# Kernel optimization log

Hardware: AMD Instinct MI355X
Metric: run time of the kernel (lower is better)

Reference implementation:

```python
import jax, jax.numpy as jnp
import numpy as np

NEG_INF = -1e30

def setup_inputs() -> dict:
    key0 = jax.random.key(0)
    kq, kk, kv, ks = jax.random.split(key0, 4)
    B, S, H, D = 4, 2048, 16, 128
    query = jax.random.normal(kq, (B, S, H, D), dtype=jnp.float32)
    key = jax.random.normal(kk, (B, S, H, D), dtype=jnp.float32)
    value = jax.random.normal(kv, (B, S, H, D), dtype=jnp.float32)
    decoder_segment_ids = jnp.sort(jax.random.randint(ks, (B, S), 0, 4), axis=-1).astype(jnp.int32)
    return {"query": query, "key": key, "value": value,
            "decoder_segment_ids": decoder_segment_ids}

def reference(query, key, value, decoder_segment_ids):
    # Splash causal attention, no 1/sqrt(d) scale (matches the wrapped kernel).
    B, S, H, D = query.shape
    # scores: [b, h, q, k]
    scores = jnp.einsum('bqhd,bkhd->bhqk', query, key)
    causal = jnp.tril(jnp.ones((S, S), dtype=bool))              # [q, k]
    seg = decoder_segment_ids
    seg_mask = seg[:, :, None] == seg[:, None, :]                # [b, q, k]
    mask = causal[None, None, :, :] & seg_mask[:, None, :, :]    # [b, 1->h, q, k]
    scores = jnp.where(mask, scores, NEG_INF)
    probs = jax.nn.softmax(scores, axis=-1)
    out = jnp.einsum('bhqk,bkhd->bqhd', probs, value)
    return out
```

## Files before the change

### kernel.cpp

```cpp
#include <hip/hip_runtime.h>
#include <hip/hip_bf16.h>

typedef short v8s __attribute__((ext_vector_type(8)));
typedef float f32x4 __attribute__((ext_vector_type(4)));

constexpr int Bb = 4, S = 2048, H = 16, Dd = 128;
constexpr int BQ = 64, BK = 32;
constexpr float NEG = -1e30f;
constexpr size_t NELEM = (size_t)Bb * S * H * Dd;

static __device__ inline short f2bs(float x) {
    __hip_bfloat16 h = __float2bfloat16(x);
    return *reinterpret_cast<short*>(&h);
}
static __device__ inline float bs2f(short s) {
    unsigned u = ((unsigned)(unsigned short)s) << 16;
    return __uint_as_float(u);
}

__global__ __launch_bounds__(256) void prep_k(const float* __restrict__ k,
                                              short* __restrict__ khi,
                                              short* __restrict__ klo) {
    size_t i = ((size_t)blockIdx.x * 256 + threadIdx.x) * 8;
    f32x4 a = *(const f32x4*)(k + i);
    f32x4 b = *(const f32x4*)(k + i + 4);
    v8s hi, lo;
#pragma unroll
    for (int j = 0; j < 4; ++j) {
        short h0 = f2bs(a[j]); hi[j] = h0;     lo[j] = f2bs(a[j] - bs2f(h0));
        short h1 = f2bs(b[j]); hi[4 + j] = h1; lo[4 + j] = f2bs(b[j] - bs2f(h1));
    }
    *(v8s*)(khi + i) = hi;
    *(v8s*)(klo + i) = lo;
}

__global__ __launch_bounds__(256) void prep_vt(const float* __restrict__ v,
                                               short* __restrict__ vt) {
    __shared__ __align__(16) short T[64][136];
    const int k0 = blockIdx.x * 64, h = blockIdx.y, b = blockIdx.z;
    const int t = threadIdx.x;
    {
        const int kk = t >> 2, c0 = (t & 3) * 32;
        const float* vb = v + (((size_t)b * S + k0 + kk) * H + h) * Dd + c0;
        short tmp[32];
#pragma unroll
        for (int j = 0; j < 32; j += 4) {
            f32x4 x = *(const f32x4*)(vb + j);
#pragma unroll
            for (int i = 0; i < 4; ++i) tmp[j + i] = f2bs(x[i]);
        }
#pragma unroll
        for (int j = 0; j < 4; ++j) *(v8s*)&T[kk][c0 + j * 8] = *(v8s*)&tmp[j * 8];
    }
    __syncthreads();
    {
        const int d = t >> 1, koff = (t & 1) * 32;
        short o16[32];
#pragma unroll
        for (int i = 0; i < 32; ++i) o16[i] = T[koff + i][d];
        short* dst = vt + ((size_t)(b * H + h) * Dd + d) * S + k0 + koff;
#pragma unroll
        for (int j = 0; j < 4; ++j) *(v8s*)(dst + j * 8) = *(v8s*)&o16[j * 8];
    }
}

__global__ __launch_bounds__(256) void fa_fast(const short* __restrict__ khi,
                                               const short* __restrict__ klo,
                                               const short* __restrict__ vtg,
                                               const float* __restrict__ q,
                                               const int* __restrict__ seg,
                                               float* __restrict__ out) {
    __shared__ __align__(16) short Khl[BK][136];
    __shared__ __align__(16) short Kll[BK][136];
    __shared__ __align__(16) short Vtl[Dd][40];
    __shared__ __align__(16) short Pl[4][16][40];

    const int qt = blockIdx.x, h = blockIdx.y, b = blockIdx.z;
    const int q0 = qt * BQ, tid = threadIdx.x;
    const int wave = tid >> 6, lane = tid & 63;
    const int quad = lane >> 4, l16 = lane & 15;

    const int rowA = q0 + wave * 16 + l16;
    const float* qbase = q + (((size_t)b * S + rowA) * H + h) * Dd;
    v8s qh[4], ql[4];
#pragma unroll
    for (int c = 0; c < 4; ++c) {
        f32x4 x0 = *(const f32x4*)(qbase + c * 32 + quad * 8);
        f32x4 x1 = *(const f32x4*)(qbase + c * 32 + quad * 8 + 4);
#pragma unroll
        for (int i = 0; i < 4; ++i) {
            short h0 = f2bs(x0[i]); qh[c][i] = h0;     ql[c][i] = f2bs(x0[i] - bs2f(h0));
            short h1 = f2bs(x1[i]); qh[c][4 + i] = h1; ql[c][4 + i] = f2bs(x1[i] - bs2f(h1));
        }
    }

    const int rowC0 = q0 + wave * 16 + quad * 4;
    const int segb = b * S;
    int segq[4];
#pragma unroll
    for (int r = 0; r < 4; ++r) segq[r] = seg[segb + rowC0 + r];
    const int seg_lo = seg[segb + q0];

    f32x4 o[8];
#pragma unroll
    for (int dt = 0; dt < 8; ++dt) o[dt] = f32x4{0.f, 0.f, 0.f, 0.f};
    float m_i[4], l_i[4];
#pragma unroll
    for (int r = 0; r < 4; ++r) { m_i[r] = NEG; l_i[r] = 0.f; }

    const int skk = tid >> 3, scol = (tid & 7) * 16;
    const int svd = tid >> 1, svo = (tid & 1) * 16;
    const size_t kbase = (((size_t)b * S + skk) * H + h) * Dd + scol;
    const size_t vbase = ((size_t)(b * H + h) * Dd + svd) * S + svo;

    const int nkt = (q0 + BQ) / BK;
    int it = 0;
    while (it < nkt && seg[segb + it * BK + BK - 1] < seg_lo) ++it;

    v8s pA, pB, pC, pD, pE, pF;
    if (it < nkt) {
        const size_t ka = kbase + (size_t)it * BK * H * Dd;
        pA = *(const v8s*)(khi + ka); pB = *(const v8s*)(khi + ka + 8);
        pC = *(const v8s*)(klo + ka); pD = *(const v8s*)(klo + ka + 8);
        const size_t va = vbase + (size_t)it * BK;
        pE = *(const v8s*)(vtg + va); pF = *(const v8s*)(vtg + va + 8);
    }

    while (it < nkt) {
        *(v8s*)&Khl[skk][scol] = pA; *(v8s*)&Khl[skk][scol + 8] = pB;
        *(v8s*)&Kll[skk][scol] = pC; *(v8s*)&Kll[skk][scol + 8] = pD;
        *(v8s*)&Vtl[svd][svo]  = pE; *(v8s*)&Vtl[svd][svo + 8]  = pF;
        __syncthreads();

        const int kt = it * BK;
        int nit = it + 1;
        while (nit < nkt && seg[segb + nit * BK + BK - 1] < seg_lo) ++nit;
        if (nit < nkt) {
            const size_t ka = kbase + (size_t)nit * BK * H * Dd;
            pA = *(const v8s*)(khi + ka); pB = *(const v8s*)(khi + ka + 8);
            pC = *(const v8s*)(klo + ka); pD = *(const v8s*)(klo + ka + 8);
            const size_t va = vbase + (size_t)nit * BK;
            pE = *(const v8s*)(vtg + va); pF = *(const v8s*)(vtg + va + 8);
        }

        float sc_[2][4];
#pragma unroll
        for (int nt = 0; nt < 2; ++nt) {
            f32x4 s = f32x4{0.f, 0.f, 0.f, 0.f};
#pragma unroll
            for (int c = 0; c < 4; ++c) {
                v8s kfh = *(const v8s*)&Khl[nt * 16 + l16][c * 32 + quad * 8];
                v8s kfl = *(const v8s*)&Kll[nt * 16 + l16][c * 32 + quad * 8];
                s = __builtin_amdgcn_mfma_f32_16x16x32_bf16(qh[c], kfh, s, 0, 0, 0);
                s = __builtin_amdgcn_mfma_f32_16x16x32_bf16(ql[c], kfh, s, 0, 0, 0);
                s = __builtin_amdgcn_mfma_f32_16x16x32_bf16(qh[c], kfl, s, 0, 0, 0);
            }
            const int kj = kt + nt * 16 + l16;
            const int sk = seg[segb + kj];
#pragma unroll
            for (int r = 0; r < 4; ++r) {
                const bool valid = (kj <= rowC0 + r) && (sk == segq[r]);
                sc_[nt][r] = valid ? s[r] : NEG;
            }
        }

        float pr[2][4];
#pragma unroll
        for (int r = 0; r < 4; ++r) {
            float mx = fmaxf(sc_[0][r], sc_[1][r]);
#pragma unroll
            for (int off = 1; off < 16; off <<= 1) mx = fmaxf(mx, __shfl_xor(mx, off));
            const float mn = fmaxf(m_i[r], mx);
            const float alpha = __expf(m_i[r] - mn);
            const float p0 = (sc_[0][r] <= 0.5f * NEG) ? 0.f : __expf(sc_[0][r] - mn);
            const float p1 = (sc_[1][r] <= 0.5f * NEG) ? 0.f : __expf(sc_[1][r] - mn);
            float rs = p0 + p1;
#pragma unroll
            for (int off = 1; off < 16; off <<= 1) rs += __shfl_xor(rs, off);
            l_i[r] = l_i[r] * alpha + rs;
            m_i[r] = mn;
#pragma unroll
            for (int dt = 0; dt < 8; ++dt) o[dt][r] *= alpha;
            pr[0][r] = p0;
            pr[1][r] = p1;
        }

#pragma unroll
        for (int nt = 0; nt < 2; ++nt)
#pragma unroll
            for (int r = 0; r < 4; ++r)
                Pl[wave][quad * 4 + r][nt * 16 + l16] = f2bs(pr[nt][r]);

        v8s pf = *(const v8s*)&Pl[wave][l16][quad * 8];
#pragma unroll
        for (int dt = 0; dt < 8; ++dt) {
            v8s vf = *(const v8s*)&Vtl[dt * 16 + l16][quad * 8];
            o[dt] = __builtin_amdgcn_mfma_f32_16x16x32_bf16(pf, vf, o[dt], 0, 0, 0);
        }
        __syncthreads();
        it = nit;
    }

    const size_t obase = (((size_t)b * S + rowC0) * H + h) * Dd;
#pragma unroll
    for (int r = 0; r < 4; ++r) {
        const float inv = 1.0f / l_i[r];
#pragma unroll
        for (int dt = 0; dt < 8; ++dt)
            out[obase + (size_t)r * H * Dd + dt * 16 + l16] = o[dt][r] * inv;
    }
}

__global__ __launch_bounds__(256) void fa_slow(const float* __restrict__ q,
                                               const float* __restrict__ k,
                                               const float* __restrict__ v,
                                               const int* __restrict__ seg,
                                               float* __restrict__ out) {
    __shared__ __align__(16) short Kh[BK][136];
    __shared__ __align__(16) short Kl[BK][136];
    __shared__ __align__(16) short Vt[Dd][40];
    __shared__ __align__(16) short Pl[4][16][40];
    const int qt = blockIdx.x, h = blockIdx.y, b = blockIdx.z;
    const int q0 = qt * BQ, tid = threadIdx.x;
    const int wave = tid >> 6, lane = tid & 63;
    const int quad = lane >> 4, l16 = lane & 15;
    const int rowA = q0 + wave * 16 + l16;
    const float* qbase = q + (((size_t)b * S + rowA) * H + h) * Dd;
    v8s qh[4], qlo[4];
#pragma unroll
    for (int c = 0; c < 4; ++c) {
        f32x4 x0 = *(const f32x4*)(qbase + c * 32 + quad * 8);
        f32x4 x1 = *(const f32x4*)(qbase + c * 32 + quad * 8 + 4);
#pragma unroll
        for (int i = 0; i < 4; ++i) {
            short h0 = f2bs(x0[i]); qh[c][i] = h0;     qlo[c][i] = f2bs(x0[i] - bs2f(h0));
            short h1 = f2bs(x1[i]); qh[c][4 + i] = h1; qlo[c][4 + i] = f2bs(x1[i] - bs2f(h1));
        }
    }
    const int rowC0 = q0 + wave * 16 + quad * 4;
    int segq[4];
#pragma unroll
    for (int r = 0; r < 4; ++r) segq[r] = seg[b * S + rowC0 + r];
    const int seg_lo = seg[b * S + q0];
    f32x4 o[8];
#pragma unroll
    for (int dt = 0; dt < 8; ++dt) o[dt] = f32x4{0.f, 0.f, 0.f, 0.f};
    float m_i[4], l_i[4];
#pragma unroll
    for (int r = 0; r < 4; ++r) { m_i[r] = NEG; l_i[r] = 0.f; }
    const int nkt = (q0 + BQ) / BK;
    for (int itx = 0; itx < nkt; ++itx) {
        const int kt = itx * BK;
        if (seg[b * S + kt + BK - 1] < seg_lo) continue;
        {
            const int kk = tid >> 3, d0 = (tid & 7) * 16;
            const float* kb = k + (((size_t)b * S + kt + kk) * H + h) * Dd + d0;
            const float* vb = v + (((size_t)b * S + kt + kk) * H + h) * Dd + d0;
#pragma unroll
            for (int j = 0; j < 4; ++j) {
                f32x4 x = *(const f32x4*)(kb + j * 4);
#pragma unroll
                for (int i = 0; i < 4; ++i) {
                    short hb = f2bs(x[i]);
                    Kh[kk][d0 + j * 4 + i] = hb;
                    Kl[kk][d0 + j * 4 + i] = f2bs(x[i] - bs2f(hb));
                }
                f32x4 y = *(const f32x4*)(vb + j * 4);
#pragma unroll
                for (int i = 0; i < 4; ++i) Vt[d0 + j * 4 + i][kk] = f2bs(y[i]);
            }
        }
        __syncthreads();
        float sc_[2][4];
#pragma unroll
        for (int nt = 0; nt < 2; ++nt) {
            f32x4 s = f32x4{0.f, 0.f, 0.f, 0.f};
#pragma unroll
            for (int c = 0; c < 4; ++c) {
                v8s kfh = *(const v8s*)&Kh[nt * 16 + l16][c * 32 + quad * 8];
                v8s kfl = *(const v8s*)&Kl[nt * 16 + l16][c * 32 + quad * 8];
                s = __builtin_amdgcn_mfma_f32_16x16x32_bf16(qh[c], kfh, s, 0, 0, 0);
                s = __builtin_amdgcn_mfma_f32_16x16x32_bf16(qlo[c], kfh, s, 0, 0, 0);
                s = __builtin_amdgcn_mfma_f32_16x16x32_bf16(qh[c], kfl, s, 0, 0, 0);
            }
            const int kj = kt + nt * 16 + l16;
            const int segk = seg[b * S + kj];
#pragma unroll
            for (int r = 0; r < 4; ++r) {
                const bool valid = (kj <= rowC0 + r) && (segk == segq[r]);
                sc_[nt][r] = valid ? s[r] : NEG;
            }
        }
        float pr[2][4];
#pragma unroll
        for (int r = 0; r < 4; ++r) {
            float mx = fmaxf(sc_[0][r], sc_[1][r]);
#pragma unroll
            for (int off = 1; off < 16; off <<= 1) mx = fmaxf(mx, __shfl_xor(mx, off));
            const float mn = fmaxf(m_i[r], mx);
            const float alpha = __expf(m_i[r] - mn);
            const float p0 = (sc_[0][r] <= 0.5f * NEG) ? 0.f : __expf(sc_[0][r] - mn);
            const float p1 = (sc_[1][r] <= 0.5f * NEG) ? 0.f : __expf(sc_[1][r] - mn);
            float rs = p0 + p1;
#pragma unroll
            for (int off = 1; off < 16; off <<= 1) rs += __shfl_xor(rs, off);
            l_i[r] = l_i[r] * alpha + rs;
            m_i[r] = mn;
#pragma unroll
            for (int dt = 0; dt < 8; ++dt) o[dt][r] *= alpha;
            pr[0][r] = p0;
            pr[1][r] = p1;
        }
#pragma unroll
        for (int nt = 0; nt < 2; ++nt)
#pragma unroll
            for (int r = 0; r < 4; ++r)
                Pl[wave][quad * 4 + r][nt * 16 + l16] = f2bs(pr[nt][r]);
        v8s pf = *(const v8s*)&Pl[wave][l16][quad * 8];
#pragma unroll
        for (int dt = 0; dt < 8; ++dt) {
            v8s vf = *(const v8s*)&Vt[dt * 16 + l16][quad * 8];
            o[dt] = __builtin_amdgcn_mfma_f32_16x16x32_bf16(pf, vf, o[dt], 0, 0, 0);
        }
        __syncthreads();
    }
    const size_t obase = (((size_t)b * S + rowC0) * H + h) * Dd;
#pragma unroll
    for (int r = 0; r < 4; ++r) {
        const float inv = 1.0f / l_i[r];
#pragma unroll
        for (int dt = 0; dt < 8; ++dt)
            out[obase + (size_t)r * H * Dd + dt * 16 + l16] = o[dt][r] * inv;
    }
}

extern "C" void kernel_launch(void* const* d_in, const int* in_sizes, int n_in,
                              void* d_out, int out_size, void* d_ws, size_t ws_size,
                              hipStream_t stream) {
    const float* q = (const float*)d_in[0];
    const float* k = (const float*)d_in[1];
    const float* v = (const float*)d_in[2];
    const int* seg = (const int*)d_in[3];
    float* out = (float*)d_out;
    const size_t need = NELEM * 2 * 3;
    dim3 grid(S / BQ, H, Bb);
    if (ws_size >= need) {
        short* khi = (short*)d_ws;
        short* klo = khi + NELEM;
        short* vtg = klo + NELEM;
        prep_k<<<(int)(NELEM / (256 * 8)), 256, 0, stream>>>(k, khi, klo);
        prep_vt<<<dim3(S / 64, H, Bb), 256, 0, stream>>>(v, vtg);
        fa_fast<<<grid, dim3(256), 0, stream>>>(khi, klo, vtg, q, seg, out);
    } else {
        fa_slow<<<grid, dim3(256), 0, stream>>>(q, k, v, seg, out);
    }
}
```

Measured before the change: 395.0 us.

## Double query rows per wave, transpose score MFMA, fuse prep kernels, reverse tile order

Merges the K split and V transpose prep kernels into one launch. The attention kernel now covers 128 query rows per block, 32 per wave, so each K/V tile staged in shared memory is reused across twice as many queries. Scores are computed transposed (K as the A operand) so the row max and row sum need only two cross-lane shuffles, and segment ids are loaded as vectors. Blocks are issued in reverse so the heavy causal tiles start first. The cost is higher register pressure from the doubled accumulators and half as many blocks.

```diff
diff --git a/kernel.cpp b/kernel.cpp
--- a/kernel.cpp
+++ b/kernel.cpp
@@ -2,10 +2,12 @@
 #include <hip/hip_bf16.h>
 
 typedef short v8s __attribute__((ext_vector_type(8)));
+typedef short v4s __attribute__((ext_vector_type(4)));
+typedef int   v4i __attribute__((ext_vector_type(4)));
 typedef float f32x4 __attribute__((ext_vector_type(4)));
 
 constexpr int Bb = 4, S = 2048, H = 16, Dd = 128;
-constexpr int BQ = 64, BK = 32;
+constexpr int BQ = 128, BK = 32;
 constexpr float NEG = -1e30f;
 constexpr size_t NELEM = (size_t)Bb * S * H * Dd;
 
@@ -18,36 +20,41 @@
     return __uint_as_float(u);
 }
 
-__global__ __launch_bounds__(256) void prep_k(const float* __restrict__ k,
-                                              short* __restrict__ khi,
-                                              short* __restrict__ klo) {
-    size_t i = ((size_t)blockIdx.x * 256 + threadIdx.x) * 8;
-    f32x4 a = *(const f32x4*)(k + i);
-    f32x4 b = *(const f32x4*)(k + i + 4);
-    v8s hi, lo;
-#pragma unroll
-    for (int j = 0; j < 4; ++j) {
-        short h0 = f2bs(a[j]); hi[j] = h0;     lo[j] = f2bs(a[j] - bs2f(h0));
-        short h1 = f2bs(b[j]); hi[4 + j] = h1; lo[4 + j] = f2bs(b[j] - bs2f(h1));
-    }
-    *(v8s*)(khi + i) = hi;
-    *(v8s*)(klo + i) = lo;
-}
-
-__global__ __launch_bounds__(256) void prep_vt(const float* __restrict__ v,
-                                               short* __restrict__ vt) {
+__global__ __launch_bounds__(256) void prep(const float* __restrict__ k,
+                                            const float* __restrict__ v,
+                                            short* __restrict__ khi,
+                                            short* __restrict__ klo,
+                                            short* __restrict__ vt) {
     __shared__ __align__(16) short T[64][136];
     const int k0 = blockIdx.x * 64, h = blockIdx.y, b = blockIdx.z;
     const int t = threadIdx.x;
+    const int kk = t >> 2, c0 = (t & 3) * 32;
+    const size_t off = (((size_t)b * S + k0 + kk) * H + h) * Dd + c0;
     {
-        const int kk = t >> 2, c0 = (t & 3) * 32;
-        const float* vb = v + (((size_t)b * S + k0 + kk) * H + h) * Dd + c0;
+        short hi[32], lo[32];
+#pragma unroll
+        for (int j = 0; j < 8; ++j) {
+            f32x4 x = *(const f32x4*)(k + off + j * 4);
+#pragma unroll
+            for (int i = 0; i < 4; ++i) {
+                short hb = f2bs(x[i]);
+                hi[j * 4 + i] = hb;
+                lo[j * 4 + i] = f2bs(x[i] - bs2f(hb));
+            }
+        }
+#pragma unroll
+        for (int j = 0; j < 4; ++j) {
+            *(v8s*)(khi + off + j * 8) = *(v8s*)&hi[j * 8];
+            *(v8s*)(klo + off + j * 8) = *(v8s*)&lo[j * 8];
+        }
+    }
+    {
         short tmp[32];
 #pragma unroll
-        for (int j = 0; j < 32; j += 4) {
-            f32x4 x = *(const f32x4*)(vb + j);
-#pragma unroll
-            for (int i = 0; i < 4; ++i) tmp[j + i] = f2bs(x[i]);
+        for (int j = 0; j < 8; ++j) {
+            f32x4 x = *(const f32x4*)(v + off + j * 4);
+#pragma unroll
+            for (int i = 0; i < 4; ++i) tmp[j * 4 + i] = f2bs(x[i]);
         }
 #pragma unroll
         for (int j = 0; j < 4; ++j) *(v8s*)&T[kk][c0 + j * 8] = *(v8s*)&tmp[j * 8];
@@ -64,54 +71,55 @@
     }
 }
 
-__global__ __launch_bounds__(256) void fa_fast(const short* __restrict__ khi,
-                                               const short* __restrict__ klo,
-                                               const short* __restrict__ vtg,
-                                               const float* __restrict__ q,
-                                               const int* __restrict__ seg,
-                                               float* __restrict__ out) {
+__global__ __launch_bounds__(256, 2) void fa2(const short* __restrict__ khi,
+                                              const short* __restrict__ klo,
+                                              const short* __restrict__ vtg,
+                                              const float* __restrict__ q,
+                                              const int* __restrict__ seg,
+                                              float* __restrict__ out) {
     __shared__ __align__(16) short Khl[BK][136];
     __shared__ __align__(16) short Kll[BK][136];
     __shared__ __align__(16) short Vtl[Dd][40];
-    __shared__ __align__(16) short Pl[4][16][40];
-
-    const int qt = blockIdx.x, h = blockIdx.y, b = blockIdx.z;
+    __shared__ __align__(16) short Pl[4][32][40];
+
+    const int qt = gridDim.x - 1 - blockIdx.x;
+    const int h = blockIdx.y, b = blockIdx.z;
     const int q0 = qt * BQ, tid = threadIdx.x;
-    const int wave = tid >> 6, lane = tid & 63;
+    const int w = tid >> 6, lane = tid & 63;
     const int quad = lane >> 4, l16 = lane & 15;
-
-    const int rowA = q0 + wave * 16 + l16;
-    const float* qbase = q + (((size_t)b * S + rowA) * H + h) * Dd;
-    v8s qh[4], ql[4];
-#pragma unroll
-    for (int c = 0; c < 4; ++c) {
-        f32x4 x0 = *(const f32x4*)(qbase + c * 32 + quad * 8);
-        f32x4 x1 = *(const f32x4*)(qbase + c * 32 + quad * 8 + 4);
-#pragma unroll
-        for (int i = 0; i < 4; ++i) {
-            short h0 = f2bs(x0[i]); qh[c][i] = h0;     ql[c][i] = f2bs(x0[i] - bs2f(h0));
-            short h1 = f2bs(x1[i]); qh[c][4 + i] = h1; ql[c][4 + i] = f2bs(x1[i] - bs2f(h1));
-        }
-    }
-
-    const int rowC0 = q0 + wave * 16 + quad * 4;
     const int segb = b * S;
-    int segq[4];
-#pragma unroll
-    for (int r = 0; r < 4; ++r) segq[r] = seg[segb + rowC0 + r];
+
+    v8s qh[2][4], ql[2][4];
+    int segq[2], qg[2];
+#pragma unroll
+    for (int m = 0; m < 2; ++m) {
+        qg[m] = q0 + w * 32 + m * 16 + l16;
+        const float* qb = q + (((size_t)b * S + qg[m]) * H + h) * Dd;
+#pragma unroll
+        for (int c = 0; c < 4; ++c) {
+            f32x4 x0 = *(const f32x4*)(qb + c * 32 + quad * 8);
+            f32x4 x1 = *(const f32x4*)(qb + c * 32 + quad * 8 + 4);
+#pragma unroll
+            for (int i = 0; i < 4; ++i) {
+                short h0 = f2bs(x0[i]); qh[m][c][i] = h0;     ql[m][c][i] = f2bs(x0[i] - bs2f(h0));
+                short h1 = f2bs(x1[i]); qh[m][c][4 + i] = h1; ql[m][c][4 + i] = f2bs(x1[i] - bs2f(h1));
+            }
+        }
+        segq[m] = seg[segb + qg[m]];
+    }
     const int seg_lo = seg[segb + q0];
 
-    f32x4 o[8];
-#pragma unroll
-    for (int dt = 0; dt < 8; ++dt) o[dt] = f32x4{0.f, 0.f, 0.f, 0.f};
-    float m_i[4], l_i[4];
-#pragma unroll
-    for (int r = 0; r < 4; ++r) { m_i[r] = NEG; l_i[r] = 0.f; }
+    f32x4 o[2][8];
+#pragma unroll
+    for (int m = 0; m < 2; ++m)
+#pragma unroll
+        for (int dt = 0; dt < 8; ++dt) o[m][dt] = f32x4{0.f, 0.f, 0.f, 0.f};
+    float m_i[2] = {NEG, NEG}, l_i[2] = {0.f, 0.f};
 
     const int skk = tid >> 3, scol = (tid & 7) * 16;
     const int svd = tid >> 1, svo = (tid & 1) * 16;
-    const size_t kbase = (((size_t)b * S + skk) * H + h) * Dd + scol;
-    const size_t vbase = ((size_t)(b * H + h) * Dd + svd) * S + svo;
+    const size_t kstage = (((size_t)b * S + skk) * H + h) * Dd + scol;
+    const size_t vstage = ((size_t)(b * H + h) * Dd + svd) * S + svo;
 
     const int nkt = (q0 + BQ) / BK;
     int it = 0;
@@ -119,10 +127,10 @@
 
     v8s pA, pB, pC, pD, pE, pF;
     if (it < nkt) {
-        const size_t ka = kbase + (size_t)it * BK * H * Dd;
+        const size_t ka = kstage + (size_t)it * BK * H * Dd;
         pA = *(const v8s*)(khi + ka); pB = *(const v8s*)(khi + ka + 8);
         pC = *(const v8s*)(klo + ka); pD = *(const v8s*)(klo + ka + 8);
-        const size_t va = vbase + (size_t)it * BK;
+        const size_t va = vstage + (size_t)it * BK;
         pE = *(const v8s*)(vtg + va); pF = *(const v8s*)(vtg + va + 8);
     }
 
@@ -136,79 +144,111 @@
         int nit = it + 1;
         while (nit < nkt && seg[segb + nit * BK + BK - 1] < seg_lo) ++nit;
         if (nit < nkt) {
-            const size_t ka = kbase + (size_t)nit * BK * H * Dd;
+            const size_t ka = kstage + (size_t)nit * BK * H * Dd;
             pA = *(const v8s*)(khi + ka); pB = *(const v8s*)(khi + ka + 8);
             pC = *(const v8s*)(klo + ka); pD = *(const v8s*)(klo + ka + 8);
-            const size_t va = vbase + (size_t)nit * BK;
+            const size_t va = vstage + (size_t)nit * BK;
             pE = *(const v8s*)(vtg + va); pF = *(const v8s*)(vtg + va + 8);
         }
 
-        float sc_[2][4];
+        v4i sk0 = *(const v4i*)(seg + segb + kt + quad * 4);
+        v4i sk1 = *(const v4i*)(seg + segb + kt + 16 + quad * 4);
+
+        float sc_[2][2][4];
 #pragma unroll
         for (int nt = 0; nt < 2; ++nt) {
-            f32x4 s = f32x4{0.f, 0.f, 0.f, 0.f};
+            v8s kfh[4], kfl[4];
 #pragma unroll
             for (int c = 0; c < 4; ++c) {
-                v8s kfh = *(const v8s*)&Khl[nt * 16 + l16][c * 32 + quad * 8];
-                v8s kfl = *(const v8s*)&Kll[nt * 16 + l16][c * 32 + quad * 8];
-                s = __builtin_amdgcn_mfma_f32_16x16x32_bf16(qh[c], kfh, s, 0, 0, 0);
-                s = __builtin_amdgcn_mfma_f32_16x16x32_bf16(ql[c], kfh, s, 0, 0, 0);
-                s = __builtin_amdgcn_mfma_f32_16x16x32_bf16(qh[c], kfl, s, 0, 0, 0);
-            }
-            const int kj = kt + nt * 16 + l16;
-            const int sk = seg[segb + kj];
+                kfh[c] = *(const v8s*)&Khl[nt * 16 + l16][c * 32 + quad * 8];
+                kfl[c] = *(const v8s*)&Kll[nt * 16 + l16][c * 32 + quad * 8];
+            }
+#pragma unroll
+            for (int m = 0; m < 2; ++m) {
+                f32x4 s = f32x4{0.f, 0.f, 0.f, 0.f};
+#pragma unroll
+                for (int c = 0; c < 4; ++c) {
+                    s = __builtin_amdgcn_mfma_f32_16x16x32_bf16(kfh[c], qh[m][c], s, 0, 0, 0);
+                    s = __builtin_amdgcn_mfma_f32_16x16x32_bf16(kfl[c], qh[m][c], s, 0, 0, 0);
+                    s = __builtin_amdgcn_mfma_f32_16x16x32_bf16(kfh[c], ql[m][c], s, 0, 0, 0);
+                }
+                const v4i skv = nt ? sk1 : sk0;
+#pragma unroll
+                for (int r = 0; r < 4; ++r) {
+                    const int kg = kt + nt * 16 + quad * 4 + r;
+                    const bool valid = (kg <= qg[m]) && (skv[r] == segq[m]);
+                    sc_[m][nt][r] = valid ? s[r] : NEG;
+                }
+            }
+        }
+
+#pragma unroll
+        for (int m = 0; m < 2; ++m) {
+            float mx = sc_[m][0][0];
+#pragma unroll
+            for (int nt = 0; nt < 2; ++nt)
+#pragma unroll
+                for (int r = 0; r < 4; ++r) mx = fmaxf(mx, sc_[m][nt][r]);
+            mx = fmaxf(mx, __shfl_xor(mx, 16));
+            mx = fmaxf(mx, __shfl_xor(mx, 32));
+            const float mn = fmaxf(m_i[m], mx);
+            const float alpha = __expf(m_i[m] - mn);
+            float pv[2][4], rs = 0.f;
+#pragma unroll
+            for (int nt = 0; nt < 2; ++nt)
+#pragma unroll
+                for (int r = 0; r < 4; ++r) {
+                    const float p = (sc_[m][nt][r] <= 0.5f * NEG) ? 0.f : __expf(sc_[m][nt][r] - mn);
+                    pv[nt][r] = p;
+                    rs += p;
+                }
+            rs += __shfl_xor(rs, 16);
+            rs += __shfl_xor(rs, 32);
+            l_i[m] = l_i[m] * alpha + rs;
+            m_i[m] = mn;
+
+#pragma unroll
+            for (int nt = 0; nt < 2; ++nt) {
+                v4s pk;
+#pragma unroll
+                for (int r = 0; r < 4; ++r) pk[r] = f2bs(pv[nt][r]);
+                *(v4s*)&Pl[w][m * 16 + l16][nt * 16 + quad * 4] = pk;
+            }
+
 #pragma unroll
             for (int r = 0; r < 4; ++r) {
-                const bool valid = (kj <= rowC0 + r) && (sk == segq[r]);
-                sc_[nt][r] = valid ? s[r] : NEG;
-            }
-        }
-
-        float pr[2][4];
-#pragma unroll
-        for (int r = 0; r < 4; ++r) {
-            float mx = fmaxf(sc_[0][r], sc_[1][r]);
-#pragma unroll
-            for (int off = 1; off < 16; off <<= 1) mx = fmaxf(mx, __shfl_xor(mx, off));
-            const float mn = fmaxf(m_i[r], mx);
-            const float alpha = __expf(m_i[r] - mn);
-            const float p0 = (sc_[0][r] <= 0.5f * NEG) ? 0.f : __expf(sc_[0][r] - mn);
-            const float p1 = (sc_[1][r] <= 0.5f * NEG) ? 0.f : __expf(sc_[1][r] - mn);
-            float rs = p0 + p1;
-#pragma unroll
-            for (int off = 1; off < 16; off <<= 1) rs += __shfl_xor(rs, off);
-            l_i[r] = l_i[r] * alpha + rs;
-            m_i[r] = mn;
-#pragma unroll
-            for (int dt = 0; dt < 8; ++dt) o[dt][r] *= alpha;
-            pr[0][r] = p0;
-            pr[1][r] = p1;
-        }
-
-#pragma unroll
-        for (int nt = 0; nt < 2; ++nt)
-#pragma unroll
-            for (int r = 0; r < 4; ++r)
-                Pl[wave][quad * 4 + r][nt * 16 + l16] = f2bs(pr[nt][r]);
-
-        v8s pf = *(const v8s*)&Pl[wave][l16][quad * 8];
+                const float ar = __shfl(alpha, (lane & 48) + quad * 4 + r);
+#pragma unroll
+                for (int dt = 0; dt < 8; ++dt) o[m][dt][r] *= ar;
+            }
+        }
+
+        v8s pf[2];
+#pragma unroll
+        for (int m = 0; m < 2; ++m) pf[m] = *(const v8s*)&Pl[w][m * 16 + l16][quad * 8];
 #pragma unroll
         for (int dt = 0; dt < 8; ++dt) {
             v8s vf = *(const v8s*)&Vtl[dt * 16 + l16][quad * 8];
-            o[dt] = __builtin_amdgcn_mfma_f32_16x16x32_bf16(pf, vf, o[dt], 0, 0, 0);
+#pragma unroll
+            for (int m = 0; m < 2; ++m)
+                o[m][dt] = __builtin_amdgcn_mfma_f32_16x16x32_bf16(pf[m], vf, o[m][dt], 0, 0, 0);
         }
         __syncthreads();
         it = nit;
     }
 
-    const size_t obase = (((size_t)b * S + rowC0) * H + h) * Dd;
-#pragma unroll
-    for (int r = 0; r < 4; ++r) {
-        const float inv = 1.0f / l_i[r];
-#pragma unroll
-        for (int dt = 0; dt < 8; ++dt)
-            out[obase + (size_t)r * H * Dd + dt * 16 + l16] = o[dt][r] * inv;
-    }
+#pragma unroll
+    for (int m = 0; m < 2; ++m)
+#pragma unroll
+        for (int r = 0; r < 4; ++r) {
+            const float lr = __shfl(l_i[m], (lane & 48) + quad * 4 + r);
+            const float inv = 1.0f / lr;
+            const int qrow = q0 + w * 32 + m * 16 + quad * 4 + r;
+            const size_t ob = (((size_t)b * S + qrow) * H + h) * Dd;
+#pragma unroll
+            for (int dt = 0; dt < 8; ++dt)
+                out[ob + dt * 16 + l16] = o[m][dt][r] * inv;
+        }
 }
 
 __global__ __launch_bounds__(256) void fa_slow(const float* __restrict__ q,
@@ -216,12 +256,12 @@
                                                const float* __restrict__ v,
                                                const int* __restrict__ seg,
                                                float* __restrict__ out) {
-    __shared__ __align__(16) short Kh[BK][136];
-    __shared__ __align__(16) short Kl[BK][136];
+    __shared__ __align__(16) short Kh[32][136];
+    __shared__ __align__(16) short Kl[32][136];
     __shared__ __align__(16) short Vt[Dd][40];
     __shared__ __align__(16) short Pl[4][16][40];
     const int qt = blockIdx.x, h = blockIdx.y, b = blockIdx.z;
-    const int q0 = qt * BQ, tid = threadIdx.x;
+    const int q0 = qt * 64, tid = threadIdx.x;
     const int wave = tid >> 6, lane = tid & 63;
     const int quad = lane >> 4, l16 = lane & 15;
     const int rowA = q0 + wave * 16 + l16;
@@ -248,10 +288,10 @@
     float m_i[4], l_i[4];
 #pragma unroll
     for (int r = 0; r < 4; ++r) { m_i[r] = NEG; l_i[r] = 0.f; }
-    const int nkt = (q0 + BQ) / BK;
+    const int nkt = (q0 + 64) / 32;
     for (int itx = 0; itx < nkt; ++itx) {
-        const int kt = itx * BK;
-        if (seg[b * S + kt + BK - 1] < seg_lo) continue;
+        const int kt = itx * 32;
+        if (seg[b * S + kt + 31] < seg_lo) continue;
         {
             const int kk = tid >> 3, d0 = (tid & 7) * 16;
             const float* kb = k + (((size_t)b * S + kt + kk) * H + h) * Dd + d0;
@@ -343,15 +383,13 @@
     const int* seg = (const int*)d_in[3];
     float* out = (float*)d_out;
     const size_t need = NELEM * 2 * 3;
-    dim3 grid(S / BQ, H, Bb);
     if (ws_size >= need) {
         short* khi = (short*)d_ws;
         short* klo = khi + NELEM;
         short* vtg = klo + NELEM;
-        prep_k<<<(int)(NELEM / (256 * 8)), 256, 0, stream>>>(k, khi, klo);
-        prep_vt<<<dim3(S / 64, H, Bb), 256, 0, stream>>>(v, vtg);
-        fa_fast<<<grid, dim3(256), 0, stream>>>(khi, klo, vtg, q, seg, out);
+        prep<<<dim3(S / 64, H, Bb), dim3(256), 0, stream>>>(k, v, khi, klo, vtg);
+        fa2<<<dim3(S / BQ, H, Bb), dim3(256), 0, stream>>>(khi, klo, vtg, q, seg, out);
     } else {
-        fa_slow<<<grid, dim3(256), 0, stream>>>(q, k, v, seg, out);
-    }
-}
+        fa_slow<<<dim3(S / 64, H, Bb), dim3(256), 0, stream>>>(q, k, v, seg, out);
+    }
+}
```

After: 334.2 us. 15.4% less time.
